# Kernel optimization log

Hardware: AMD Instinct MI355X
Metric: run time of the kernel (lower is better)

The kernel has to match this reference:

```python
import jax, jax.numpy as jnp
import numpy as np

B_, S_, H_, I_, N_, K_ = 2, 2048, 1024, 2048, 16, 4

def setup_inputs() -> dict:
    key = jax.random.key(0)
    ks = jax.random.split(key, 6)
    return {
        "x": jax.random.normal(ks[0], (B_, S_, H_), jnp.float32),
        "W_in": jax.random.normal(ks[1], (H_, 2 * I_), jnp.float32) * (H_ ** -0.5),
        "conv_w": jax.random.normal(ks[2], (I_, 1, K_), jnp.float32) * (K_ ** -0.5),
        "ln_gamma": jnp.ones((I_,), jnp.float32),
        "ln_beta": jnp.zeros((I_,), jnp.float32),
        "W_xproj": jax.random.normal(ks[3], (I_, 2 * N_ + 1), jnp.float32) * (I_ ** -0.5),
        "A_param": jax.random.normal(ks[4], (I_, N_), jnp.float32) * 0.1,
        "D": jnp.ones((I_,), jnp.float32),
        "W_out": jax.random.normal(ks[5], (I_, H_), jnp.float32) * (I_ ** -0.5),
    }

def _layernorm(x, g, b, eps=1e-5):
    mu = jnp.mean(x, axis=-1, keepdims=True)
    var = jnp.mean((x - mu) ** 2, axis=-1, keepdims=True)
    return (x - mu) * jax.lax.rsqrt(var + eps) * g + b

def reference(x, W_in, conv_w, ln_gamma, ln_beta, W_xproj, A_param, D, W_out):
    b, s, _ = x.shape
    n = A_param.shape[1]
    xz = x @ W_in                                   # (b,s,2I)
    xc, z = jnp.split(xz, 2, axis=-1)
    # depthwise causal conv1d: torch pads both sides k-1 then truncates [:s] == left-pad k-1
    xc = jax.lax.conv_general_dilated(
        xc.transpose(0, 2, 1), conv_w, window_strides=(1,),
        padding=[(conv_w.shape[-1] - 1, 0)],
        feature_group_count=conv_w.shape[0],
        dimension_numbers=("NCH", "OIH", "NCH")).transpose(0, 2, 1)  # (b,s,I)
    xc = jax.nn.silu(xc)
    xc = _layernorm(xc, ln_gamma, ln_beta)
    xp = xc @ W_xproj                               # (b,s,2N+1)
    delta = jnp.clip(jax.nn.softplus(xp[..., :1]), 1e-6, 10.0)   # (b,s,1)
    Bm = xp[..., 1:1 + n]                           # (b,s,N)
    Cm = xp[..., 1 + n:]                            # (b,s,N)
    A = -jnp.clip(jax.nn.softplus(A_param), 0.1, 10.0)           # (I,N)
    # decay[b,s,i,n] = exp(delta[b,s] * A[i,n]), clamped
    decay = jnp.clip(jnp.exp(delta[..., None] * A[None, None]), 1e-6, 1.0)  # (b,s,I,N)
    # y = x * sum_n B*C*decay  (state-dim reduction of the broadcast 4D tensor)
    y = xc * jnp.einsum("bsn,bsin->bsi", Bm * Cm, decay)
    y = y + xc * D
    return (y * jax.nn.silu(z)) @ W_out
```

## Files before the change

kernel.cpp:

```cpp
#include <hip/hip_runtime.h>
#include <hip/hip_bf16.h>
#include <cmath>

typedef __bf16 bf16_t;
typedef __bf16 bf16x8 __attribute__((ext_vector_type(8)));
typedef __bf16 bf16x4 __attribute__((ext_vector_type(4)));
typedef float  f32x4  __attribute__((ext_vector_type(4)));

static constexpr int B_  = 2, S_ = 2048, H_ = 1024, I_ = 2048, NST = 16;
static constexpr int ROWS  = B_ * S_;
static constexpr int TWO_I = 2 * I_;
static constexpr int XPD   = 2 * NST + 1;
static constexpr int XPN   = 64;

#define AS_G(p) ((const __attribute__((address_space(1))) void*)(p))
#define AS_L(p) ((__attribute__((address_space(3))) void*)(p))

template<int N> __device__ __forceinline__ void wait_vmcnt();
template<> __device__ __forceinline__ void wait_vmcnt<4>() {
    asm volatile("s_waitcnt vmcnt(4)" ::: "memory");
}

__device__ __forceinline__ float softplus_f(float x) {
    return x > 15.f ? x : log1pf(__expf(x));
}

__device__ __forceinline__ f32x4 b2f(bf16x4 v) {
    return (f32x4){(float)v[0], (float)v[1], (float)v[2], (float)v[3]};
}

__device__ __forceinline__ float fast_exp2(float x) {
#if __has_builtin(__builtin_amdgcn_exp2f)
    return __builtin_amdgcn_exp2f(x);
#else
    return exp2f(x);
#endif
}
__device__ __forceinline__ float fast_rcp(float x) {
#if __has_builtin(__builtin_amdgcn_rcpf)
    return __builtin_amdgcn_rcpf(x);
#else
    return 1.f / x;
#endif
}
__device__ __forceinline__ float fast_sigmoid(float x) {
    return fast_rcp(1.f + __expf(-x));
}
__device__ __forceinline__ float rflf(float x) {
    return __int_as_float(__builtin_amdgcn_readfirstlane(__float_as_int(x)));
}

template<int GX, int GY, int XW>
__device__ __forceinline__ void xcd_swz(int id, int& bx, int& by) {
    constexpr int SX = GX / XW;
    constexpr int SY = GY * XW / 8;
    const int xcd = id & 7;
    const int j   = id >> 3;
    bx = (xcd % XW) * SX + j % SX;
    by = (xcd / XW) * SY + j / SX;
}


__global__ __launch_bounds__(256)
void prep_all(const float* __restrict__ x, const float* __restrict__ W_in,
              const float* __restrict__ W_out, const float* __restrict__ A_param,
              const float* __restrict__ Wx, const float* __restrict__ conv_w,
              bf16_t* __restrict__ Xb, bf16_t* __restrict__ W1t,
              bf16_t* __restrict__ Wot, float* __restrict__ A2T,
              float* __restrict__ cwT, bf16_t* __restrict__ WxTb)
{
    const int b   = blockIdx.x;
    const int tid = threadIdx.x;
    __shared__ float t[32][33];

    if (b < 4096) {
        const int i = b * 256 + tid;
        f32x4 v = *(const f32x4*)(x + (size_t)i * 4);
        bf16x4 o;
        o[0] = (bf16_t)v[0]; o[1] = (bf16_t)v[1];
        o[2] = (bf16_t)v[2]; o[3] = (bf16_t)v[3];
        *(bf16x4*)(Xb + (size_t)i * 4) = o;
    } else if (b < 8192) {
        const int tb = b - 4096;
        const int c0 = (tb & 127) * 32, r0 = (tb >> 7) * 32;
        const int tx = tid & 31, ty = tid >> 5;
        #pragma unroll
        for (int k = 0; k < 4; ++k)
            t[ty + 8 * k][tx] = W_in[(size_t)(r0 + ty + 8 * k) * 4096 + c0 + tx];
        __syncthreads();
        #pragma unroll
        for (int k = 0; k < 4; ++k)
            W1t[(size_t)(c0 + ty + 8 * k) * 1024 + r0 + tx] = (bf16_t)t[tx][ty + 8 * k];
    } else if (b < 10240) {
        const int tb = b - 8192;
        const int c0 = (tb & 31) * 32, r0 = (tb >> 5) * 32;
        const int tx = tid & 31, ty = tid >> 5;
        #pragma unroll
        for (int k = 0; k < 4; ++k)
            t[ty + 8 * k][tx] = W_out[(size_t)(r0 + ty + 8 * k) * 1024 + c0 + tx];
        __syncthreads();
        #pragma unroll
        for (int k = 0; k < 4; ++k)
            Wot[(size_t)(c0 + ty + 8 * k) * 2048 + r0 + tx] = (bf16_t)t[tx][ty + 8 * k];
    } else {
        const int i = (b - 10240) * 256 + tid;
        if (i < NST * I_) {
            int n = i >> 11, c = i & (I_ - 1);
            float sp = softplus_f(A_param[(size_t)c * NST + n]);
            A2T[i] = -fminf(fmaxf(sp, 0.1f), 10.f) * 1.44269504088896340736f;
        }
        if (i < 4 * I_) {
            int j = i >> 11, c = i & (I_ - 1);
            cwT[i] = conv_w[(size_t)c * 4 + j];
        }
        if (i < XPN * I_) {
            int j = i >> 11, c = i & (I_ - 1);
            WxTb[i] = (j < XPD) ? (bf16_t)Wx[(size_t)c * XPD + j] : (bf16_t)0.f;
        }
    }
}


template<int M, int N, int K, int BM, int BN, int WM, int WN, int THREADS,
         int GX, int GY, int XW, typename OutT>
__global__ __launch_bounds__(THREADS)
void gemm_fp(const bf16_t* __restrict__ A, const bf16_t* __restrict__ Bt,
             OutT* __restrict__ C)
{
    constexpr int BK  = 32;
    constexpr int NT  = K / BK;
    constexpr int MR  = BM / WM / 16;
    constexpr int NR  = BN / WN / 16;
    constexpr int MH  = MR / 2;
    constexpr int RPC = THREADS / 4;
    constexpr int CA  = BM / RPC;
    constexpr int CB  = BN / RPC;
    constexpr int CT  = CA + CB;
    static_assert(CT == 4, "vmcnt template fixed at 4");

    __shared__ bf16_t lA[4][BM * BK];
    __shared__ bf16_t lB[4][BN * BK];

    int bx, by;
    xcd_swz<GX, GY, XW>(blockIdx.x, bx, by);
    const int bm = by * BM;
    const int bn = bx * BN;

    const int tid  = threadIdx.x;
    const int lane = tid & 63;
    const int wave = tid >> 6;
    const int wm   = wave / WN;
    const int wn   = wave % WN;

    const int frow = lane & 15;
    const int fsw  = ((lane >> 4) ^ ((frow >> 1) & 3)) << 3;

    const int str = tid >> 2;
    const int stp = tid & 3;

    const bf16_t* baseA[CA];
    #pragma unroll
    for (int a = 0; a < CA; ++a) {
        const int rt = a * RPC + str;
        baseA[a] = A + (size_t)(bm + rt) * K + ((stp ^ ((rt >> 1) & 3)) << 3);
    }
    const bf16_t* baseB[CB];
    #pragma unroll
    for (int a = 0; a < CB; ++a) {
        const int rt = a * RPC + str;
        baseB[a] = Bt + (size_t)(bn + rt) * K + ((stp ^ ((rt >> 1) & 3)) << 3);
    }

    f32x4 acc[MR][NR];
    #pragma unroll
    for (int m = 0; m < MR; ++m)
        #pragma unroll
        for (int n = 0; n < NR; ++n)
            acc[m][n] = (f32x4){0.f, 0.f, 0.f, 0.f};

    auto stageA = [&](int k0, int b) {
        #pragma unroll
        for (int a = 0; a < CA; ++a)
            __builtin_amdgcn_global_load_lds(AS_G(baseA[a] + k0),
                AS_L(&lA[b][a * RPC * 32 + wave * 512]), 16, 0, 0);
    };
    auto stageB = [&](int k0, int b) {
        #pragma unroll
        for (int a = 0; a < CB; ++a)
            __builtin_amdgcn_global_load_lds(AS_G(baseB[a] + k0),
                AS_L(&lB[b][a * RPC * 32 + wave * 512]), 16, 0, 0);
    };

    stageA(0, 0); stageB(0, 0);
    stageA(BK, 1); stageB(BK, 1);
    wait_vmcnt<4>();
    __builtin_amdgcn_s_barrier();

    #pragma unroll 1
    for (int t = 0; t < NT; ++t) {
        const int buf = t & 3;
        const int nb  = (t + 2) & 3;
        int kn = (t + 2) * BK;
        if (kn >= K) kn -= K;

        bf16x8 bfr[NR];
        #pragma unroll
        for (int n = 0; n < NR; ++n)
            bfr[n] = *(const bf16x8*)(&lB[buf][(wn * (NR * 16) + n * 16 + frow) * 32 + fsw]);
        bf16x8 af0[MH];
        #pragma unroll
        for (int m = 0; m < MH; ++m)
            af0[m] = *(const bf16x8*)(&lA[buf][(wm * (MR * 16) + m * 16 + frow) * 32 + fsw]);
        stageA(kn, nb);

        __builtin_amdgcn_s_setprio(1);
        #pragma unroll
        for (int m = 0; m < MH; ++m)
            #pragma unroll
            for (int n = 0; n < NR; ++n)
                acc[m][n] = __builtin_amdgcn_mfma_f32_16x16x32_bf16(
                    af0[m], bfr[n], acc[m][n], 0, 0, 0);
        __builtin_amdgcn_s_setprio(0);

        bf16x8 af1[MR - MH];
        #pragma unroll
        for (int m = 0; m < MR - MH; ++m)
            af1[m] = *(const bf16x8*)(&lA[buf][(wm * (MR * 16) + (MH + m) * 16 + frow) * 32 + fsw]);
        stageB(kn, nb);

        __builtin_amdgcn_s_setprio(1);
        #pragma unroll
        for (int m = 0; m < MR - MH; ++m)
            #pragma unroll
            for (int n = 0; n < NR; ++n)
                acc[MH + m][n] = __builtin_amdgcn_mfma_f32_16x16x32_bf16(
                    af1[m], bfr[n], acc[MH + m][n], 0, 0, 0);
        __builtin_amdgcn_s_setprio(0);

        wait_vmcnt<4>();
        __builtin_amdgcn_s_barrier();
    }

    const int crow = (lane >> 4) * 4;
    const int ccol = lane & 15;
    #pragma unroll
    for (int m = 0; m < MR; ++m)
        #pragma unroll
        for (int n = 0; n < NR; ++n)
            #pragma unroll
            for (int r = 0; r < 4; ++r)
                C[(size_t)(bm + wm * (MR * 16) + m * 16 + crow + r) * N
                  + (bn + wn * (NR * 16) + n * 16 + ccol)] = (OutT)acc[m][n][r];
}


__global__ __launch_bounds__(256)
void conv_ln(const bf16_t* __restrict__ xz,
             const float* __restrict__ cwT,
             const float* __restrict__ ln_g,
             const float* __restrict__ ln_b,
             bf16_t* __restrict__ Xn)
{
    const int row  = blockIdx.x;
    const int s    = row & (S_ - 1);
    const int tid  = threadIdx.x;
    const int lane = tid & 63;
    const int wave = tid >> 6;
    const bf16_t* xzr = xz + (size_t)row * TWO_I;

    __shared__ float lnr[4][2];

    float xc[8];
    float sm = 0.f, sq = 0.f;

    #pragma unroll
    for (int g = 0; g < 2; ++g) {
        const int c = g * 1024 + tid * 4;
        const f32x4 w0 = *(const f32x4*)(cwT + 0 * I_ + c);
        const f32x4 w1 = *(const f32x4*)(cwT + 1 * I_ + c);
        const f32x4 w2 = *(const f32x4*)(cwT + 2 * I_ + c);
        const f32x4 w3 = *(const f32x4*)(cwT + 3 * I_ + c);
        const f32x4 z4 = (f32x4){0.f, 0.f, 0.f, 0.f};
        const f32x4 xv0 = (s >= 3) ? b2f(*(const bf16x4*)(xzr - 3 * TWO_I + c)) : z4;
        const f32x4 xv1 = (s >= 2) ? b2f(*(const bf16x4*)(xzr - 2 * TWO_I + c)) : z4;
        const f32x4 xv2 = (s >= 1) ? b2f(*(const bf16x4*)(xzr - 1 * TWO_I + c)) : z4;
        const f32x4 xv3 = b2f(*(const bf16x4*)(xzr + c));
        const f32x4 a = w0 * xv0 + w1 * xv1 + w2 * xv2 + w3 * xv3;
        #pragma unroll
        for (int e = 0; e < 4; ++e) {
            const float v = a[e];
            const float t = v * fast_sigmoid(v);
            xc[g * 4 + e] = t;
            sm += t; sq += t * t;
        }
    }

    #pragma unroll
    for (int off = 32; off; off >>= 1) {
        sm += __shfl_xor(sm, off, 64);
        sq += __shfl_xor(sq, off, 64);
    }
    if (lane == 0) { lnr[wave][0] = sm; lnr[wave][1] = sq; }
    __syncthreads();
    sm = lnr[0][0] + lnr[1][0] + lnr[2][0] + lnr[3][0];
    sq = lnr[0][1] + lnr[1][1] + lnr[2][1] + lnr[3][1];
    const float mu = sm * (1.f / I_);
    const float rs = rsqrtf(sq * (1.f / I_) - mu * mu + 1e-5f);

    #pragma unroll
    for (int g = 0; g < 2; ++g) {
        const int c = g * 1024 + tid * 4;
        const f32x4 gg = *(const f32x4*)(ln_g + c);
        const f32x4 bb = *(const f32x4*)(ln_b + c);
        bf16x4 h4;
        #pragma unroll
        for (int e = 0; e < 4; ++e)
            h4[e] = (bf16_t)((xc[g * 4 + e] - mu) * rs * gg[e] + bb[e]);
        *(bf16x4*)(Xn + (size_t)row * I_ + c) = h4;
    }
}


__global__ __launch_bounds__(256)
void xproj_gemm(const bf16_t* __restrict__ Xn,
                const bf16_t* __restrict__ Wb, float* __restrict__ xp_part)
{
    constexpr int BM = 128, BK = 32, KS = 512;
    __shared__ bf16_t lA[BM * BK];
    __shared__ bf16_t lB[XPN * BK];

    const int bm   = blockIdx.x * BM;
    const int ks   = blockIdx.y;
    const int tid  = threadIdx.x;
    const int lane = tid & 63;
    const int wave = tid >> 6;
    const int wm   = (wave >> 1) * 64;
    const int wn   = (wave & 1) * 32;

    const int srow  = lane >> 2;
    const int skoff = (lane & 3) * 8;
    const int frow  = lane & 15;
    const int fko   = (lane >> 4) * 8;

    f32x4 acc[4][2];
    #pragma unroll
    for (int m = 0; m < 4; ++m)
        #pragma unroll
        for (int n = 0; n < 2; ++n)
            acc[m][n] = (f32x4){0.f, 0.f, 0.f, 0.f};

    for (int k0 = ks * KS; k0 < ks * KS + KS; k0 += BK) {
        #pragma unroll
        for (int t = 0; t < 2; ++t) {
            const int c = wave * 2 + t;
            const bf16_t* ga = Xn + (size_t)(bm + c * 16 + srow) * I_ + k0 + skoff;
            __builtin_amdgcn_global_load_lds(AS_G(ga), AS_L(lA + c * 512), 16, 0, 0);
        }
        const bf16_t* gb = Wb + (size_t)(wave * 16 + srow) * I_ + k0 + skoff;
        __builtin_amdgcn_global_load_lds(AS_G(gb), AS_L(lB + wave * 512), 16, 0, 0);
        __syncthreads();

        bf16x8 af[4], bf2[2];
        #pragma unroll
        for (int m = 0; m < 4; ++m)
            af[m] = *(const bf16x8*)(lA + (wm + m * 16 + frow) * BK + fko);
        #pragma unroll
        for (int n = 0; n < 2; ++n)
            bf2[n] = *(const bf16x8*)(lB + (wn + n * 16 + frow) * BK + fko);

        #pragma unroll
        for (int m = 0; m < 4; ++m)
            #pragma unroll
            for (int n = 0; n < 2; ++n)
                acc[m][n] = __builtin_amdgcn_mfma_f32_16x16x32_bf16(
                    af[m], bf2[n], acc[m][n], 0, 0, 0);

        __syncthreads();
    }

    float* out = xp_part + ((size_t)ks * ROWS + bm) * XPN;
    const int crow = (lane >> 4) * 4;
    const int ccol = lane & 15;
    #pragma unroll
    for (int m = 0; m < 4; ++m)
        #pragma unroll
        for (int n = 0; n < 2; ++n)
            #pragma unroll
            for (int r = 0; r < 4; ++r)
                out[(size_t)(wm + m * 16 + crow + r) * XPN
                    + (wn + n * 16 + ccol)] = acc[m][n][r];
}


__global__ __launch_bounds__(256)
void ssm_gate(const bf16_t* __restrict__ xz,
              const bf16_t* __restrict__ Xn,
              const float* __restrict__ xp_part,
              const float* __restrict__ A2T,
              const float* __restrict__ Dv,
              bf16_t* __restrict__ U)
{
    const int row0 = blockIdx.x * 2;
    const int tid  = threadIdx.x;

    __shared__ float xps[2][XPD];
    __shared__ float bcs[2][NST];

    if (tid < XPD) {
        float s = 0.f;
        #pragma unroll
        for (int ks = 0; ks < 4; ++ks)
            s += xp_part[((size_t)ks * ROWS + row0) * XPN + tid];
        xps[0][tid] = s;
    } else if (tid >= 64 && tid < 64 + XPD) {
        const int j = tid - 64;
        float s = 0.f;
        #pragma unroll
        for (int ks = 0; ks < 4; ++ks)
            s += xp_part[((size_t)ks * ROWS + row0 + 1) * XPN + j];
        xps[1][j] = s;
    }
    __syncthreads();
    if (tid < NST)
        bcs[0][tid] = xps[0][1 + tid] * xps[0][1 + NST + tid];
    else if (tid >= 64 && tid < 64 + NST) {
        const int n = tid - 64;
        bcs[1][n] = xps[1][1 + n] * xps[1][1 + NST + n];
    }
    __syncthreads();

    const float d0 = fminf(fmaxf(softplus_f(xps[0][0]), 1e-6f), 10.f);
    const float d1 = fminf(fmaxf(softplus_f(xps[1][0]), 1e-6f), 10.f);

    const bf16_t* z0 = xz + (size_t)row0 * TWO_I + I_;
    const bf16_t* z1 = z0 + TWO_I;
    bf16_t* u0 = U + (size_t)row0 * I_;
    bf16_t* u1 = u0 + I_;

    #pragma unroll 1
    for (int g = 0; g < 2; ++g) {
        const int c = g * 1024 + tid * 4;
        f32x4 sa0 = (f32x4){0.f, 0.f, 0.f, 0.f};
        f32x4 sa1 = (f32x4){0.f, 0.f, 0.f, 0.f};
        #pragma unroll 1
        for (int nb = 0; nb < 4; ++nb) {
            const float* ap = A2T + (size_t)(nb * 4) * I_ + c;
            const f32x4 a0 = *(const f32x4*)(ap);
            const f32x4 a1 = *(const f32x4*)(ap + I_);
            const f32x4 a2 = *(const f32x4*)(ap + 2 * I_);
            const f32x4 a3 = *(const f32x4*)(ap + 3 * I_);
            const float b00 = rflf(bcs[0][nb * 4 + 0]), b10 = rflf(bcs[1][nb * 4 + 0]);
            const float b01 = rflf(bcs[0][nb * 4 + 1]), b11 = rflf(bcs[1][nb * 4 + 1]);
            const float b02 = rflf(bcs[0][nb * 4 + 2]), b12 = rflf(bcs[1][nb * 4 + 2]);
            const float b03 = rflf(bcs[0][nb * 4 + 3]), b13 = rflf(bcs[1][nb * 4 + 3]);
            #pragma unroll
            for (int e = 0; e < 4; ++e) {
                sa0[e] += b00 * fast_exp2(d0 * a0[e]);
                sa1[e] += b10 * fast_exp2(d1 * a0[e]);
                sa0[e] += b01 * fast_exp2(d0 * a1[e]);
                sa1[e] += b11 * fast_exp2(d1 * a1[e]);
                sa0[e] += b02 * fast_exp2(d0 * a2[e]);
                sa1[e] += b12 * fast_exp2(d1 * a2[e]);
                sa0[e] += b03 * fast_exp2(d0 * a3[e]);
                sa1[e] += b13 * fast_exp2(d1 * a3[e]);
            }
        }
        const f32x4 dvv = *(const f32x4*)(Dv + c);
        const f32x4 xn0 = b2f(*(const bf16x4*)(Xn + (size_t)row0 * I_ + c));
        const f32x4 xn1 = b2f(*(const bf16x4*)(Xn + (size_t)(row0 + 1) * I_ + c));
        const f32x4 zv0 = b2f(*(const bf16x4*)(z0 + c));
        const f32x4 zv1 = b2f(*(const bf16x4*)(z1 + c));
        bf16x4 o0, o1;
        #pragma unroll
        for (int e = 0; e < 4; ++e) {
            const float y0 = xn0[e] * (sa0[e] + dvv[e]);
            const float y1 = xn1[e] * (sa1[e] + dvv[e]);
            const float zz0 = zv0[e], zz1 = zv1[e];
            o0[e] = (bf16_t)(y0 * zz0 * fast_sigmoid(zz0));
            o1[e] = (bf16_t)(y1 * zz1 * fast_sigmoid(zz1));
        }
        *(bf16x4*)(u0 + c) = o0;
        *(bf16x4*)(u1 + c) = o1;
    }
}


extern "C" void kernel_launch(void* const* d_in, const int* in_sizes, int n_in,
                              void* d_out, int out_size, void* d_ws, size_t ws_size,
                              hipStream_t stream)
{
    const float* x     = (const float*)d_in[0];
    const float* W_in  = (const float*)d_in[1];
    const float* convw = (const float*)d_in[2];
    const float* ln_g  = (const float*)d_in[3];
    const float* ln_b  = (const float*)d_in[4];
    const float* Wx    = (const float*)d_in[5];
    const float* A_p   = (const float*)d_in[6];
    const float* Dv    = (const float*)d_in[7];
    const float* W_out = (const float*)d_in[8];
    float* out = (float*)d_out;

    char* ws = (char*)d_ws;
    bf16_t* Xb   = (bf16_t*)(ws);
    bf16_t* W1t  = (bf16_t*)(ws + (size_t)(8u  << 20));
    bf16_t* Wot  = (bf16_t*)(ws + (size_t)(16u << 20));
    float*  A2T  = (float*) (ws + (size_t)(20u << 20));
    float*  cwT  = (float*) (ws + (size_t)(20u << 20) + (128u << 10));
    bf16_t* WxTb = (bf16_t*)(ws + (size_t)(20u << 20) + (256u << 10));
    bf16_t* XZb  = (bf16_t*)(ws + (size_t)(22u << 20));
    bf16_t* U    = (bf16_t*)(ws + (size_t)(54u << 20));
    bf16_t* Xn   = (bf16_t*)(ws);
    float*  xp4  = (float*) (ws + (size_t)(86u << 20));

    prep_all<<<10752, 256, 0, stream>>>(x, W_in, W_out, A_p, Wx, convw,
                                        Xb, W1t, Wot, A2T, cwT, WxTb);

    gemm_fp<ROWS, TWO_I, H_, 256, 256, 2, 4, 512, 16, 16, 4, bf16_t>
        <<<256, 512, 0, stream>>>(Xb, W1t, XZb);
    conv_ln<<<ROWS, 256, 0, stream>>>(XZb, cwT, ln_g, ln_b, Xn);
    xproj_gemm<<<dim3(ROWS / 128, 4), 256, 0, stream>>>(Xn, WxTb, xp4);
    ssm_gate<<<ROWS / 2, 256, 0, stream>>>(XZb, Xn, xp4, A2T, Dv, U);
    gemm_fp<ROWS, H_, I_, 128, 128, 2, 2, 256, 8, 32, 2, float>
        <<<256, 256, 0, stream>>>(U, Wot, out);
}
```

Measured before the change: 141.9 us.

## Split K across two wave groups in output GEMM with LDS reduction

```diff
diff --git a/kernel.cpp b/kernel.cpp
--- a/kernel.cpp
+++ b/kernel.cpp
@@ -135,8 +135,7 @@
     constexpr int RPC = THREADS / 4;
     constexpr int CA  = BM / RPC;
     constexpr int CB  = BN / RPC;
-    constexpr int CT  = CA + CB;
-    static_assert(CT == 4, "vmcnt template fixed at 4");
+    static_assert(CA + CB == 4, "vmcnt template fixed at 4");
 
     __shared__ bf16_t lA[4][BM * BK];
     __shared__ bf16_t lB[4][BN * BK];
@@ -251,6 +250,160 @@
             for (int r = 0; r < 4; ++r)
                 C[(size_t)(bm + wm * (MR * 16) + m * 16 + crow + r) * N
                   + (bn + wn * (NR * 16) + n * 16 + ccol)] = (OutT)acc[m][n][r];
+}
+
+
+template<int M, int N, int K, int GX, int GY, int XW>
+__global__ __launch_bounds__(512)
+void gemm3_kg(const bf16_t* __restrict__ A, const bf16_t* __restrict__ Bt,
+              float* __restrict__ C)
+{
+    constexpr int BM = 128, BN = 128, BK = 32;
+    constexpr int KH = K / 2;
+    constexpr int NT = KH / BK;
+    constexpr int MR = 4, NR = 4, MH = 2;
+
+    __shared__ bf16_t smem[65536];
+
+    int bx, by;
+    xcd_swz<GX, GY, XW>(blockIdx.x, bx, by);
+    const int bm = by * BM;
+    const int bn = bx * BN;
+
+    const int tid  = threadIdx.x;
+    const int lane = tid & 63;
+    const int wave = tid >> 6;
+    const int grp  = wave >> 2;
+    const int gw   = wave & 3;
+    const int wm   = gw >> 1;
+    const int wn   = gw & 1;
+
+    const int frow = lane & 15;
+    const int fsw  = ((lane >> 4) ^ ((frow >> 1) & 3)) << 3;
+
+    const int gtid = tid & 255;
+    const int str  = gtid >> 2;
+    const int stp  = gtid & 3;
+
+    bf16_t* lA = smem + grp * 16384;
+    bf16_t* lB = smem + 32768 + grp * 16384;
+
+    const bf16_t* baseA[2];
+    #pragma unroll
+    for (int a = 0; a < 2; ++a) {
+        const int rt = a * 64 + str;
+        baseA[a] = A + (size_t)(bm + rt) * K + grp * KH + ((stp ^ ((rt >> 1) & 3)) << 3);
+    }
+    const bf16_t* baseB[2];
+    #pragma unroll
+    for (int a = 0; a < 2; ++a) {
+        const int rt = a * 64 + str;
+        baseB[a] = Bt + (size_t)(bn + rt) * K + grp * KH + ((stp ^ ((rt >> 1) & 3)) << 3);
+    }
+
+    f32x4 acc[MR][NR];
+    #pragma unroll
+    for (int m = 0; m < MR; ++m)
+        #pragma unroll
+        for (int n = 0; n < NR; ++n)
+            acc[m][n] = (f32x4){0.f, 0.f, 0.f, 0.f};
+
+    auto stageA = [&](int k0, int b) {
+        #pragma unroll
+        for (int a = 0; a < 2; ++a)
+            __builtin_amdgcn_global_load_lds(AS_G(baseA[a] + k0),
+                AS_L(lA + b * 4096 + a * 2048 + gw * 512), 16, 0, 0);
+    };
+    auto stageB = [&](int k0, int b) {
+        #pragma unroll
+        for (int a = 0; a < 2; ++a)
+            __builtin_amdgcn_global_load_lds(AS_G(baseB[a] + k0),
+                AS_L(lB + b * 4096 + a * 2048 + gw * 512), 16, 0, 0);
+    };
+
+    stageA(0, 0); stageB(0, 0);
+    stageA(BK, 1); stageB(BK, 1);
+    wait_vmcnt<4>();
+    __builtin_amdgcn_s_barrier();
+
+    #pragma unroll 1
+    for (int t = 0; t < NT; ++t) {
+        const int buf = t & 3;
+        const int nb  = (t + 2) & 3;
+        int kn = (t + 2) * BK;
+        if (kn >= KH) kn -= KH;
+
+        bf16x8 bfr[NR];
+        #pragma unroll
+        for (int n = 0; n < NR; ++n)
+            bfr[n] = *(const bf16x8*)(lB + buf * 4096 + (wn * 64 + n * 16 + frow) * 32 + fsw);
+        bf16x8 af0[MH];
+        #pragma unroll
+        for (int m = 0; m < MH; ++m)
+            af0[m] = *(const bf16x8*)(lA + buf * 4096 + (wm * 64 + m * 16 + frow) * 32 + fsw);
+        stageA(kn, nb);
+
+        __builtin_amdgcn_s_setprio(1);
+        #pragma unroll
+        for (int m = 0; m < MH; ++m)
+            #pragma unroll
+            for (int n = 0; n < NR; ++n)
+                acc[m][n] = __builtin_amdgcn_mfma_f32_16x16x32_bf16(
+                    af0[m], bfr[n], acc[m][n], 0, 0, 0);
+        __builtin_amdgcn_s_setprio(0);
+
+        bf16x8 af1[MR - MH];
+        #pragma unroll
+        for (int m = 0; m < MR - MH; ++m)
+            af1[m] = *(const bf16x8*)(lA + buf * 4096 + (wm * 64 + (MH + m) * 16 + frow) * 32 + fsw);
+        stageB(kn, nb);
+
+        __builtin_amdgcn_s_setprio(1);
+        #pragma unroll
+        for (int m = 0; m < MR - MH; ++m)
+            #pragma unroll
+            for (int n = 0; n < NR; ++n)
+                acc[MH + m][n] = __builtin_amdgcn_mfma_f32_16x16x32_bf16(
+                    af1[m], bfr[n], acc[MH + m][n], 0, 0, 0);
+        __builtin_amdgcn_s_setprio(0);
+
+        wait_vmcnt<4>();
+        __builtin_amdgcn_s_barrier();
+    }
+
+    asm volatile("s_waitcnt vmcnt(0)" ::: "memory");
+    __builtin_amdgcn_s_barrier();
+
+    float* accx = (float*)smem;
+    const int crow = (lane >> 4) * 4;
+    const int ccol = lane & 15;
+
+    if (grp == 1) {
+        #pragma unroll
+        for (int m = 0; m < MR; ++m)
+            #pragma unroll
+            for (int n = 0; n < NR; ++n) {
+                const int row = wm * 64 + m * 16 + crow;
+                const int col = wn * 64 + n * 16 + ccol;
+                #pragma unroll
+                for (int r = 0; r < 4; ++r)
+                    accx[(size_t)(row + r) * 132 + col] = acc[m][n][r];
+            }
+    }
+    __syncthreads();
+    if (grp == 0) {
+        #pragma unroll
+        for (int m = 0; m < MR; ++m)
+            #pragma unroll
+            for (int n = 0; n < NR; ++n) {
+                const int row = wm * 64 + m * 16 + crow;
+                const int col = wn * 64 + n * 16 + ccol;
+                #pragma unroll
+                for (int r = 0; r < 4; ++r)
+                    C[(size_t)(bm + row + r) * N + bn + col] =
+                        acc[m][n][r] + accx[(size_t)(row + r) * 132 + col];
+            }
+    }
 }
 
 
@@ -520,6 +673,6 @@
     conv_ln<<<ROWS, 256, 0, stream>>>(XZb, cwT, ln_g, ln_b, Xn);
     xproj_gemm<<<dim3(ROWS / 128, 4), 256, 0, stream>>>(Xn, WxTb, xp4);
     ssm_gate<<<ROWS / 2, 256, 0, stream>>>(XZb, Xn, xp4, A2T, Dv, U);
-    gemm_fp<ROWS, H_, I_, 128, 128, 2, 2, 256, 8, 32, 2, float>
-        <<<256, 256, 0, stream>>>(U, Wot, out);
-}
+    gemm3_kg<ROWS, H_, I_, 8, 32, 2>
+        <<<256, 512, 0, stream>>>(U, Wot, out);
+}
```

New measurement: 125.0 us. -11.9%, faster.
